# Kernel tuning notes

Measured on AMD Instinct MI355X. Metric: run time of the kernel, lower is better.

## Reference

```python
import jax, jax.numpy as jnp
import numpy as np

N = 1_000_000
D = 128          # weights_dim
F = 128          # feat_in_channels
G = 512          # num graphs in batch


def setup_inputs() -> dict:
    key = jax.random.key(0)
    k1, k2, k3, k4, k5 = jax.random.split(key, 5)
    weights_x = jax.random.normal(k1, (N, D), dtype=jnp.float32)
    feats_x = jax.random.normal(k2, (N, F), dtype=jnp.float32)
    W_fc = jax.random.normal(k3, (2 * D, D), dtype=jnp.float32) * (1.0 / np.sqrt(D))
    W_attn = jax.random.normal(k4, (1, 2 * D + F), dtype=jnp.float32) * (1.0 / np.sqrt(2 * D + F))
    segment_ids = jnp.sort(jax.random.randint(k5, (N,), 0, G, dtype=jnp.int32))
    return {"weights_x": weights_x, "feats_x": feats_x, "W_fc": W_fc,
            "W_attn": W_attn, "segment_ids": segment_ids, "num_graphs": G}


def reference(weights_x, feats_x, W_fc, W_attn, segment_ids, num_graphs):
    # readout_fc: [N, D] -> [N, 2D], no bias
    out = weights_x @ W_fc.T
    # hstack with additional feats -> [N, 2D + F]
    out = jnp.concatenate([out, feats_x], axis=-1)
    # attn fc -> [N, 1], then LeakyReLU(0.1)
    score = out @ W_attn.T
    score = jnp.where(score >= 0, score, 0.1 * score)
    # segment (per-graph) softmax over nodes
    seg_max = jax.ops.segment_max(score, segment_ids, num_segments=num_graphs)  # [G,1]
    e = jnp.exp(score - seg_max[segment_ids])
    seg_sum = jax.ops.segment_sum(e, segment_ids, num_segments=num_graphs)      # [G,1]
    soft = e / seg_sum[segment_ids]
    # scale by mean number of nodes per graph (batch_num_nodes().float().mean())
    counts = jax.ops.segment_sum(jnp.ones((score.shape[0],), dtype=jnp.float32),
                                 segment_ids, num_segments=num_graphs)          # [G]
    return soft * jnp.mean(counts)
```

## Files before the change

### kernel.cpp

```cpp
#include <hip/hip_runtime.h>
#include <math.h>


#define GCAP 8192

__device__ __forceinline__ unsigned fkey(float f) {
  unsigned u = __float_as_uint(f);
  return (u & 0x80000000u) ? ~u : (u | 0x80000000u);
}
__device__ __forceinline__ float funkey(unsigned k) {
  unsigned u = (k & 0x80000000u) ? (k & 0x7fffffffu) : ~k;
  return __uint_as_float(u);
}

__global__ void init_kernel(const float* __restrict__ W_fc, const float* __restrict__ W_attn,
                            const int* __restrict__ num_graphs,
                            float* __restrict__ v, unsigned* __restrict__ segmax,
                            float* __restrict__ segsum) {
  const int t = threadIdx.x;
  const int G = *num_graphs;
  for (int i = t; i < G; i += blockDim.x) { segmax[i] = 0u; segsum[i] = 0.0f; }
  if (t < 128) {
    float acc = 0.0f;
    for (int j = 0; j < 256; ++j) acc += W_fc[j * 128 + t] * W_attn[j];
    v[t] = acc;
  }
}

__global__ void score_kernel(const float* __restrict__ wx, const float* __restrict__ fx,
                             const int* __restrict__ seg, const float* __restrict__ v,
                             const float* __restrict__ W_attn,
                             float* __restrict__ score, unsigned* __restrict__ segmax,
                             int N) {
  const int lane = threadIdx.x & 63;
  const int wid  = (blockIdx.x * blockDim.x + threadIdx.x) >> 6;
  const int nW   = (gridDim.x * blockDim.x) >> 6;
  const int chunk = (N + nW - 1) / nW;
  const int n0 = wid * chunk;
  const int n1 = min(n0 + chunk, N);
  if (n0 >= N) return;

  const float2 vv = ((const float2*)v)[lane];
  const float2 ww = ((const float2*)(W_attn + 256))[lane];

  int   curSeg = -1;
  float curMax = 0.0f;
  for (int n = n0; n < n1; ++n) {
    const float2 x = ((const float2*)(wx + (size_t)n * 128))[lane];
    const float2 f = ((const float2*)(fx + (size_t)n * 128))[lane];
    float p = x.x * vv.x + x.y * vv.y + f.x * ww.x + f.y * ww.y;
#pragma unroll
    for (int off = 32; off; off >>= 1) p += __shfl_xor(p, off);
    const float s = (p >= 0.0f) ? p : 0.1f * p;
    if (lane == 0) score[n] = s;
    const int sg = seg[n];
    if (sg != curSeg) {
      if (curSeg >= 0 && lane == 0) atomicMax(&segmax[curSeg], fkey(curMax));
      curSeg = sg;
      curMax = s;
    } else {
      curMax = fmaxf(curMax, s);
    }
  }
  if (curSeg >= 0 && lane == 0) atomicMax(&segmax[curSeg], fkey(curMax));
}

__global__ void exp_kernel(const float* __restrict__ score, const int* __restrict__ seg,
                           const unsigned* __restrict__ segmax,
                           float* __restrict__ e, float* __restrict__ segsum, int N) {
  const int n    = blockIdx.x * blockDim.x + threadIdx.x;
  const int lane = threadIdx.x & 63;
  const int nc   = min(n, N - 1);
  const int sg   = seg[nc];
  const float s  = score[nc];
  const float m  = funkey(segmax[sg]);
  const float ev = (n < N) ? expf(s - m) : 0.0f;
  if (n < N) e[n] = ev;

  const int sg0 = __shfl(sg, 0);
  if (__all(sg == sg0)) {
    float sum = ev;
#pragma unroll
    for (int off = 32; off; off >>= 1) sum += __shfl_xor(sum, off);
    if (lane == 0) atomicAdd(&segsum[sg0], sum);
  } else if (n < N) {
    atomicAdd(&segsum[sg], ev);
  }
}

__global__ void out_kernel(const float* __restrict__ e, const int* __restrict__ seg,
                           const float* __restrict__ segsum,
                           const int* __restrict__ num_graphs,
                           float* __restrict__ out, int N) {
  const int n = blockIdx.x * blockDim.x + threadIdx.x;
  if (n >= N) return;
  const float scale = (float)N / (float)(*num_graphs);
  out[n] = (e[n] / segsum[seg[n]]) * scale;
}

extern "C" void kernel_launch(void* const* d_in, const int* in_sizes, int n_in,
                              void* d_out, int out_size, void* d_ws, size_t ws_size,
                              hipStream_t stream) {
  const float* wx     = (const float*)d_in[0];
  const float* fx     = (const float*)d_in[1];
  const float* W_fc   = (const float*)d_in[2];
  const float* W_attn = (const float*)d_in[3];
  const int*   seg    = (const int*)d_in[4];
  const int*   nGptr  = (const int*)d_in[5];
  float*       out    = (float*)d_out;
  const int N = in_sizes[0] / 128;

  char* ws = (char*)d_ws;
  float*    v      = (float*)ws;
  unsigned* segmax = (unsigned*)(ws + 1024);
  float*    segsum = (float*)(ws + 1024 + 4 * GCAP);

  init_kernel<<<1, 256, 0, stream>>>(W_fc, W_attn, nGptr, v, segmax, segsum);

  score_kernel<<<2048, 256, 0, stream>>>(wx, fx, seg, v, W_attn, out, segmax, N);

  const int nb = (N + 255) / 256;
  exp_kernel<<<nb, 256, 0, stream>>>(out, seg, segmax, out, segsum, N);
  out_kernel<<<nb, 256, 0, stream>>>(out, seg, segsum, nGptr, out, N);
}
```

Measured before the change: 1.063 ms.

## Process two rows per wavefront with float4 nontemporal loads; split segment max into separate kernel

The score kernel now handles two nodes per wavefront iteration, with each half-wave reading one 512-byte row as float4 using nontemporal loads. It only writes scores, and a new warp-reduced segmax kernel computes the per-segment maxima afterwards. This widens the memory accesses and takes the segment tracking and atomics out of the bandwidth-bound loop. The cost is one extra kernel launch and another 4 MB pass over the scores and segment ids.

```diff
diff --git a/kernel.cpp b/kernel.cpp
--- a/kernel.cpp
+++ b/kernel.cpp
@@ -3,6 +3,8 @@
 
 
 #define GCAP 8192
+
+typedef float f4 __attribute__((ext_vector_type(4)));
 
 __device__ __forceinline__ unsigned fkey(float f) {
   unsigned u = __float_as_uint(f);
@@ -28,41 +30,54 @@
 }
 
 __global__ void score_kernel(const float* __restrict__ wx, const float* __restrict__ fx,
-                             const int* __restrict__ seg, const float* __restrict__ v,
-                             const float* __restrict__ W_attn,
-                             float* __restrict__ score, unsigned* __restrict__ segmax,
-                             int N) {
+                             const float* __restrict__ v, const float* __restrict__ W_attn,
+                             float* __restrict__ score, int N) {
   const int lane = threadIdx.x & 63;
+  const int q    = lane & 31;
+  const int half = lane >> 5;
   const int wid  = (blockIdx.x * blockDim.x + threadIdx.x) >> 6;
   const int nW   = (gridDim.x * blockDim.x) >> 6;
-  const int chunk = (N + nW - 1) / nW;
-  const int n0 = wid * chunk;
-  const int n1 = min(n0 + chunk, N);
-  if (n0 >= N) return;
+  const int pairs = (N + 1) >> 1;
+  const int chunk = (pairs + nW - 1) / nW;
+  const int p0 = wid * chunk;
+  const int p1 = min(p0 + chunk, pairs);
 
-  const float2 vv = ((const float2*)v)[lane];
-  const float2 ww = ((const float2*)(W_attn + 256))[lane];
+  const f4 vv = ((const f4*)v)[q];
+  const f4 ww = ((const f4*)(W_attn + 256))[q];
 
-  int   curSeg = -1;
-  float curMax = 0.0f;
-  for (int n = n0; n < n1; ++n) {
-    const float2 x = ((const float2*)(wx + (size_t)n * 128))[lane];
-    const float2 f = ((const float2*)(fx + (size_t)n * 128))[lane];
-    float p = x.x * vv.x + x.y * vv.y + f.x * ww.x + f.y * ww.y;
+#pragma unroll 2
+  for (int p = p0; p < p1; ++p) {
+    const size_t base = (size_t)p * 256;
+    const f4 x = __builtin_nontemporal_load(&((const f4*)(wx + base))[lane]);
+    const f4 f = __builtin_nontemporal_load(&((const f4*)(fx + base))[lane]);
+    float s = x.x * vv.x + x.y * vv.y + x.z * vv.z + x.w * vv.w
+            + f.x * ww.x + f.y * ww.y + f.z * ww.z + f.w * ww.w;
 #pragma unroll
-    for (int off = 32; off; off >>= 1) p += __shfl_xor(p, off);
-    const float s = (p >= 0.0f) ? p : 0.1f * p;
-    if (lane == 0) score[n] = s;
-    const int sg = seg[n];
-    if (sg != curSeg) {
-      if (curSeg >= 0 && lane == 0) atomicMax(&segmax[curSeg], fkey(curMax));
-      curSeg = sg;
-      curMax = s;
-    } else {
-      curMax = fmaxf(curMax, s);
+    for (int off = 1; off < 32; off <<= 1) s += __shfl_xor(s, off);
+    s = (s >= 0.0f) ? s : 0.1f * s;
+    const int n = 2 * p + half;
+    if (q == 0 && n < N) score[n] = s;
+  }
+}
+
+__global__ void segmax_kernel(const float* __restrict__ score, const int* __restrict__ seg,
+                              unsigned* __restrict__ segmax, int N) {
+  const int n    = blockIdx.x * blockDim.x + threadIdx.x;
+  const int lane = threadIdx.x & 63;
+  const int nc   = min(n, N - 1);
+  const int sg   = seg[nc];
+  unsigned k = (n < N) ? fkey(score[nc]) : 0u;
+  const int sg0 = __shfl(sg, 0);
+  if (__all(sg == sg0)) {
+#pragma unroll
+    for (int off = 32; off; off >>= 1) {
+      unsigned o = (unsigned)__shfl_xor((int)k, off);
+      k = k > o ? k : o;
     }
+    if (lane == 0) atomicMax(&segmax[sg0], k);
+  } else if (n < N) {
+    atomicMax(&segmax[sg], k);
   }
-  if (curSeg >= 0 && lane == 0) atomicMax(&segmax[curSeg], fkey(curMax));
 }
 
 __global__ void exp_kernel(const float* __restrict__ score, const int* __restrict__ seg,
@@ -117,9 +132,10 @@
 
   init_kernel<<<1, 256, 0, stream>>>(W_fc, W_attn, nGptr, v, segmax, segsum);
 
-  score_kernel<<<2048, 256, 0, stream>>>(wx, fx, seg, v, W_attn, out, segmax, N);
+  score_kernel<<<2048, 256, 0, stream>>>(wx, fx, v, W_attn, out, N);
 
   const int nb = (N + 255) / 256;
+  segmax_kernel<<<nb, 256, 0, stream>>>(out, seg, segmax, N);
   exp_kernel<<<nb, 256, 0, stream>>>(out, seg, segmax, out, segsum, N);
   out_kernel<<<nb, 256, 0, stream>>>(out, seg, segsum, nGptr, out, N);
 }
```

Result: faster. 1.021 ms (-4.0%).
